# Kernel tuning notes

Measured on AMD Instinct MI355X. Metric: run time of the kernel, lower is better.

The kernel has to match this reference:

```python
import jax, jax.numpy as jnp
import numpy as np

DET = 512       # detector bins
N_THETA = 180   # projection angles, theta = 0..179 degrees (1 deg spacing)


def _ramp_filter(size):
    """skimage _get_fourier_filter(size, 'ramp'): spatial ramp -> FFT."""
    n = np.concatenate((np.arange(1, size // 2 + 1, 2),
                        np.arange(size // 2 - 1, 0, -2)))
    f = np.zeros(size)
    f[0] = 0.25
    f[1::2] = -1.0 / (np.pi * n) ** 2
    return jnp.asarray(2.0 * np.real(np.fft.fft(f)), dtype=jnp.float32)


def _iradon(x):
    B, C, det, A = x.shape
    theta = jnp.deg2rad(jnp.arange(A, dtype=jnp.float32))  # 0..179 deg

    # --- ramp filtering along the detector axis ---
    size = max(64, int(2 ** np.ceil(np.log2(2 * det))))  # 1024 for det=512
    filt = _ramp_filter(size)                            # (size,)
    xp = jnp.pad(x, ((0, 0), (0, 0), (0, size - det), (0, 0)))
    proj_f = jnp.fft.fft(xp, axis=2) * filt[None, None, :, None]
    filtered = jnp.real(jnp.fft.ifft(proj_f, axis=2))[:, :, :det, :]  # (B,C,det,A)

    # --- backprojection (circle=False) ---
    out_size = int(np.floor(np.sqrt(det ** 2 / 2.0)))  # 362
    radius = out_size // 2
    xpr = jnp.arange(out_size, dtype=jnp.float32)[:, None] - radius  # rows
    ypr = jnp.arange(out_size, dtype=jnp.float32)[None, :] - radius  # cols
    cos_t = jnp.cos(theta)
    sin_t = jnp.sin(theta)
    # detector coordinate for every (angle, pixel): t = y*cos - x*sin
    t = ypr[None] * cos_t[:, None, None] - xpr[None] * sin_t[:, None, None]  # (A,out,out)
    pos = t + det // 2          # index into detector axis (x = arange(det)-det//2)
    i0 = jnp.floor(pos).astype(jnp.int32)
    frac = pos - i0.astype(jnp.float32)
    in_range = ((pos >= 0) & (pos <= det - 1)).astype(jnp.float32)  # fill_value=0 outside
    i0c = jnp.clip(i0, 0, det - 1)
    i1c = jnp.clip(i0 + 1, 0, det - 1)

    P = out_size * out_size
    ft = jnp.moveaxis(filtered, 3, 2)                     # (B,C,A,det)
    idx0 = jnp.broadcast_to(i0c.reshape(A, P)[None, None], (B, C, A, P))
    idx1 = jnp.broadcast_to(i1c.reshape(A, P)[None, None], (B, C, A, P))
    g0 = jnp.take_along_axis(ft, idx0, axis=3)            # (B,C,A,P)
    g1 = jnp.take_along_axis(ft, idx1, axis=3)
    w = frac.reshape(A, P)[None, None]
    m = in_range.reshape(A, P)[None, None]
    val = ((1.0 - w) * g0 + w * g1) * m                   # bilinear-in-1D interp, 0 outside
    recon = val.sum(axis=2).reshape(B, C, out_size, out_size)
    return recon * (jnp.pi / (2.0 * A))


def setup_inputs() -> dict:
    key = jax.random.key(0)
    x = jax.random.normal(key, (4, 1, DET, N_THETA), dtype=jnp.float32)
    return {"x": x}


def reference(x):
    return _iradon(x)
```

## Files before the change

### kernel.cpp

```cpp
#include <hip/hip_runtime.h>
#include <math.h>

#define DET 512
#define NA  180
#define OUT 362
#define RAD 181

#define NSPLIT 6
#define APB    30
#define CHUNK  6
#define LSTRIDE 516

constexpr double PI_D = 3.14159265358979323846;

constexpr double tsin(double x) {
    double x2 = x * x;
    return x * (1.0 + x2 * (-1.0/6 + x2 * (1.0/120 + x2 * (-1.0/5040 +
               x2 * (1.0/362880 + x2 * (-1.0/39916800))))));
}
constexpr double tcos(double x) {
    double x2 = x * x;
    return 1.0 + x2 * (-0.5 + x2 * (1.0/24 + x2 * (-1.0/720 +
               x2 * (1.0/40320 + x2 * (-1.0/3628800)))));
}

struct Trig { float c[NA]; float s[NA]; };
constexpr Trig make_trig() {
    Trig t{};
    constexpr double r = PI_D / 180.0;
    for (int k = 0; k < NA; ++k) {
        double c, s;
        if (k <= 45)       { c =  tcos(k * r);          s =  tsin(k * r); }
        else if (k <= 90)  { c =  tsin((90 - k) * r);   s =  tcos((90 - k) * r); }
        else if (k <= 135) { c = -tsin((k - 90) * r);   s =  tcos((k - 90) * r); }
        else               { c = -tcos((180 - k) * r);  s =  tsin((180 - k) * r); }
        t.c[k] = (float)c; t.s[k] = (float)s;
    }
    return t;
}
__device__ constexpr Trig TRIG = make_trig();

__host__ __device__ constexpr float rampw0(int m) {
    int a = m < 0 ? -m : m;
    if (a > 511 || (a & 1) == 0) return 0.0f;
    double md = (double)a;
    return (float)(-2.0 / (PI_D * PI_D * md * md));
}

template<int R>
__device__ __forceinline__ void tap(const float* __restrict__ p,
        float& a0, float& a1, float& a2, float& a3) {
    const float v = p[R];
    if constexpr (rampw0(R)      != 0.0f) a0 = fmaf(rampw0(R),      v, a0);
    if constexpr (rampw0(R - 32) != 0.0f) a1 = fmaf(rampw0(R - 32), v, a1);
    if constexpr (rampw0(R - 64) != 0.0f) a2 = fmaf(rampw0(R - 64), v, a2);
    if constexpr (rampw0(R - 96) != 0.0f) a3 = fmaf(rampw0(R - 96), v, a3);
}

template<int R, int REND>
__device__ __forceinline__ void sweep(const float* __restrict__ p,
        float& a0, float& a1, float& a2, float& a3) {
    if constexpr (R <= REND) {
        tap<R>(p, a0, a1, a2, a3);
        sweep<R + 2, REND>(p, a0, a1, a2, a3);
    }
}

__global__ __launch_bounds__(256) void ramp_filter_kernel(
        const float* __restrict__ x, float* __restrict__ ft) {
    const int a   = blockIdx.x;
    const int b   = blockIdx.y;
    const int tid = threadIdx.x;
    const int t    = tid & 127;
    const int half = tid >> 7;
    const int q = (t & 31) + 128 * (t >> 5);

    __shared__ float xs[3 * DET];
    __shared__ float red[4 * 128];

    xs[tid]        = 0.0f;
    xs[256 + tid]  = 0.0f;
    xs[1024 + tid] = 0.0f;
    xs[1280 + tid] = 0.0f;
    xs[512 + tid]  = x[(b * DET + tid) * NA + a];
    xs[768 + tid]  = x[(b * DET + 256 + tid) * NA + a];
    __syncthreads();

    const float* p = xs + 512 + q;
    float a0 = 0.0f, a1 = 0.0f, a2 = 0.0f, a3 = 0.0f;

    if (half == 0) {
        a0 = 0.5f * p[0];
        a1 = 0.5f * p[32];
        a2 = 0.5f * p[64];
        a3 = 0.5f * p[96];
        sweep<-511, 47>(p, a0, a1, a2, a3);
    } else {
        sweep<49, 607>(p, a0, a1, a2, a3);
        red[      t] = a0;
        red[128 + t] = a1;
        red[256 + t] = a2;
        red[384 + t] = a3;
    }
    __syncthreads();

    if (half == 0) {
        float* o = ft + (b * NA + a) * DET + q;
        o[0]  = a0 + red[      t];
        o[32] = a1 + red[128 + t];
        o[64] = a2 + red[256 + t];
        o[96] = a3 + red[384 + t];
    }
}

__device__ __forceinline__ float interp1(const float* __restrict__ L, float pos) {
    float pf = floorf(pos);
    int   i0 = (int)pf;
    float fr = pos - pf;
    float g0 = L[i0];
    float g1 = L[i0 + 1];
    float v  = fmaf(fr, g1 - g0, g0);
    return pos <= (float)(DET - 1) ? v : 0.0f;
}

__global__ __launch_bounds__(256, 8) void backproject_kernel(
        const float* __restrict__ ft, float* __restrict__ out) {
    const int bz = blockIdx.z;
    const int b  = bz / NSPLIT;
    const int sp = bz - b * NSPLIT;
    const int r0 = blockIdx.y * 32;
    const int c0 = blockIdx.x * 32;
    const int tid = threadIdx.x;
    const int tx = tid & 15;
    const int ty = tid >> 4;

    __shared__ float line[CHUNK * LSTRIDE];

    if (tid < CHUNK) line[tid * LSTRIDE + 512] = 0.0f;

    const float xpr = (float)(min(r0 + ty, OUT - 1) - RAD);
    const float ypr = (float)(min(c0 + tx, OUT - 1) - RAD);

    float a00 = 0.0f, a01 = 0.0f, a10 = 0.0f, a11 = 0.0f;

    const float* base = ft + (b * NA + sp * APB) * DET;

    for (int rd = 0; rd < APB / CHUNK; ++rd) {
        __syncthreads();
        const float4* g = (const float4*)(base + rd * CHUNK * DET);
        #pragma unroll
        for (int k = 0; k < (CHUNK * DET / 4) / 256; ++k) {
            int j4 = tid + k * 256;
            float4 v = g[j4];
            int c = j4 >> 7;
            int d = (j4 & 127) << 2;
            *(float4*)&line[c * LSTRIDE + d] = v;
        }
        __syncthreads();

        const int abase = sp * APB + rd * CHUNK;
        #pragma unroll
        for (int i = 0; i < CHUNK; ++i) {
            const float cv = TRIG.c[abase + i];
            const float sv = TRIG.s[abase + i];
            float p00 = fmaf(ypr, cv, fmaf(xpr, -sv, 256.0f));
            float p01 = fmaf(16.0f, cv, p00);
            float p10 = fmaf(-16.0f, sv, p00);
            float p11 = fmaf(-16.0f, sv, p01);
            const float* L = line + i * LSTRIDE;
            a00 += interp1(L, p00);
            a01 += interp1(L, p01);
            a10 += interp1(L, p10);
            a11 += interp1(L, p11);
        }
    }

    const float scale = (float)(PI_D / (2.0 * NA));
    const int r = r0 + ty;
    const int c = c0 + tx;
    float* ob = out + b * OUT * OUT;
    if (r < OUT) {
        if (c < OUT)      atomicAdd(&ob[r * OUT + c],      a00 * scale);
        if (c + 16 < OUT) atomicAdd(&ob[r * OUT + c + 16], a01 * scale);
    }
    if (r + 16 < OUT) {
        if (c < OUT)      atomicAdd(&ob[(r + 16) * OUT + c],      a10 * scale);
        if (c + 16 < OUT) atomicAdd(&ob[(r + 16) * OUT + c + 16], a11 * scale);
    }
}

extern "C" void kernel_launch(void* const* d_in, const int* in_sizes, int n_in,
                              void* d_out, int out_size, void* d_ws, size_t ws_size,
                              hipStream_t stream) {
    const float* x = (const float*)d_in[0];
    float* ft  = (float*)d_ws;
    float* out = (float*)d_out;

    const int B = in_sizes[0] / (DET * NA);

    hipMemsetAsync(out, 0, (size_t)out_size * sizeof(float), stream);
    ramp_filter_kernel<<<dim3(NA, B), 256, 0, stream>>>(x, ft);
    backproject_kernel<<<dim3((OUT + 31) / 32, (OUT + 31) / 32, B * NSPLIT),
                         256, 0, stream>>>(ft, out);
}
```

Baseline: 98.49 us.

## Interleave batch into float4 detector lines and split ramp filter four ways

The filtered sinogram is now stored batch-interleaved as float4 (angle, detector, batch), so each backprojection thread computes its interpolation position and index once and serves all four batch images with one 16-byte LDS load per tap. The angle split grows to 12 blocks per tile (each with 15 angles in chunks of 5), and the batch dimension leaves the grid. The ramp filter moves to 512 threads, splitting the tap sweep into four quarters with a three-way shared reduction. In exchange the batch size is hardcoded to 4, accumulator and LDS pressure rise, and the out-of-range check now redirects loads to a zero-padded slot.

```diff
diff --git a/kernel.cpp b/kernel.cpp
--- a/kernel.cpp
+++ b/kernel.cpp
@@ -5,11 +5,13 @@
 #define NA  180
 #define OUT 362
 #define RAD 181
-
-#define NSPLIT 6
-#define APB    30
-#define CHUNK  6
-#define LSTRIDE 516
+#define OUTSQ (OUT * OUT)
+#define NB  4
+
+#define NSPLIT 12
+#define APB    15
+#define CHUNK  5
+#define LQ     514
 
 constexpr double PI_D = 3.14159265358979323846;
 
@@ -66,95 +68,97 @@
     }
 }
 
-__global__ __launch_bounds__(256) void ramp_filter_kernel(
+__global__ __launch_bounds__(512) void ramp_filter_kernel(
         const float* __restrict__ x, float* __restrict__ ft) {
     const int a   = blockIdx.x;
     const int b   = blockIdx.y;
     const int tid = threadIdx.x;
-    const int t    = tid & 127;
-    const int half = tid >> 7;
+    const int t   = tid & 127;
+    const int qtr = tid >> 7;
     const int q = (t & 31) + 128 * (t >> 5);
 
     __shared__ float xs[3 * DET];
-    __shared__ float red[4 * 128];
+    __shared__ float red[3][4][128];
 
     xs[tid]        = 0.0f;
-    xs[256 + tid]  = 0.0f;
     xs[1024 + tid] = 0.0f;
-    xs[1280 + tid] = 0.0f;
     xs[512 + tid]  = x[(b * DET + tid) * NA + a];
-    xs[768 + tid]  = x[(b * DET + 256 + tid) * NA + a];
     __syncthreads();
 
     const float* p = xs + 512 + q;
     float a0 = 0.0f, a1 = 0.0f, a2 = 0.0f, a3 = 0.0f;
 
-    if (half == 0) {
+    if (qtr == 0) {
         a0 = 0.5f * p[0];
         a1 = 0.5f * p[32];
         a2 = 0.5f * p[64];
         a3 = 0.5f * p[96];
-        sweep<-511, 47>(p, a0, a1, a2, a3);
+        sweep<-511, -233>(p, a0, a1, a2, a3);
+    } else if (qtr == 1) {
+        sweep<-231, 47>(p, a0, a1, a2, a3);
+    } else if (qtr == 2) {
+        sweep<49, 327>(p, a0, a1, a2, a3);
     } else {
-        sweep<49, 607>(p, a0, a1, a2, a3);
-        red[      t] = a0;
-        red[128 + t] = a1;
-        red[256 + t] = a2;
-        red[384 + t] = a3;
+        sweep<329, 607>(p, a0, a1, a2, a3);
+    }
+    if (qtr != 0) {
+        red[qtr - 1][0][t] = a0;
+        red[qtr - 1][1][t] = a1;
+        red[qtr - 1][2][t] = a2;
+        red[qtr - 1][3][t] = a3;
     }
     __syncthreads();
 
-    if (half == 0) {
-        float* o = ft + (b * NA + a) * DET + q;
-        o[0]  = a0 + red[      t];
-        o[32] = a1 + red[128 + t];
-        o[64] = a2 + red[256 + t];
-        o[96] = a3 + red[384 + t];
-    }
-}
-
-__device__ __forceinline__ float interp1(const float* __restrict__ L, float pos) {
+    if (qtr == 0) {
+        float* ob = ft + ((size_t)a * DET + q) * NB + b;
+        ob[0 * 4 * NB / 4 * 0] = 0.0f;
+        ob[0]        = a0 + red[0][0][t] + red[1][0][t] + red[2][0][t];
+        ob[32 * NB]  = a1 + red[0][1][t] + red[1][1][t] + red[2][1][t];
+        ob[64 * NB]  = a2 + red[0][2][t] + red[1][2][t] + red[2][2][t];
+        ob[96 * NB]  = a3 + red[0][3][t] + red[1][3][t] + red[2][3][t];
+    }
+}
+
+__device__ __forceinline__ void acc4(float4& acc,
+        const float4* __restrict__ L, float pos) {
     float pf = floorf(pos);
+    float fr = pos - pf;
     int   i0 = (int)pf;
-    float fr = pos - pf;
-    float g0 = L[i0];
-    float g1 = L[i0 + 1];
-    float v  = fmaf(fr, g1 - g0, g0);
-    return pos <= (float)(DET - 1) ? v : 0.0f;
-}
-
-__global__ __launch_bounds__(256, 8) void backproject_kernel(
-        const float* __restrict__ ft, float* __restrict__ out) {
-    const int bz = blockIdx.z;
-    const int b  = bz / NSPLIT;
-    const int sp = bz - b * NSPLIT;
+    const float4* q = (pos > (float)(DET - 1)) ? (L + DET) : (L + i0);
+    float4 g0 = q[0];
+    float4 g1 = q[1];
+    acc.x += fmaf(fr, g1.x - g0.x, g0.x);
+    acc.y += fmaf(fr, g1.y - g0.y, g0.y);
+    acc.z += fmaf(fr, g1.z - g0.z, g0.z);
+    acc.w += fmaf(fr, g1.w - g0.w, g0.w);
+}
+
+__global__ __launch_bounds__(256) void backproject_kernel(
+        const float4* __restrict__ ftq, float* __restrict__ out) {
+    const int sp = blockIdx.z;
     const int r0 = blockIdx.y * 32;
     const int c0 = blockIdx.x * 32;
     const int tid = threadIdx.x;
     const int tx = tid & 15;
     const int ty = tid >> 4;
 
-    __shared__ float line[CHUNK * LSTRIDE];
-
-    if (tid < CHUNK) line[tid * LSTRIDE + 512] = 0.0f;
+    __shared__ float4 lines[CHUNK][LQ];
+
+    if (tid < 2 * CHUNK)
+        lines[tid >> 1][DET + (tid & 1)] = float4{0.0f, 0.0f, 0.0f, 0.0f};
 
     const float xpr = (float)(min(r0 + ty, OUT - 1) - RAD);
     const float ypr = (float)(min(c0 + tx, OUT - 1) - RAD);
 
-    float a00 = 0.0f, a01 = 0.0f, a10 = 0.0f, a11 = 0.0f;
-
-    const float* base = ft + (b * NA + sp * APB) * DET;
+    float4 a00 = {0,0,0,0}, a01 = {0,0,0,0}, a10 = {0,0,0,0}, a11 = {0,0,0,0};
 
     for (int rd = 0; rd < APB / CHUNK; ++rd) {
         __syncthreads();
-        const float4* g = (const float4*)(base + rd * CHUNK * DET);
+        const float4* g = ftq + (size_t)(sp * APB + rd * CHUNK) * DET;
         #pragma unroll
-        for (int k = 0; k < (CHUNK * DET / 4) / 256; ++k) {
-            int j4 = tid + k * 256;
-            float4 v = g[j4];
-            int c = j4 >> 7;
-            int d = (j4 & 127) << 2;
-            *(float4*)&line[c * LSTRIDE + d] = v;
+        for (int k = 0; k < CHUNK * DET / 256; ++k) {
+            int j = tid + k * 256;
+            lines[j >> 9][j & 511] = g[j];
         }
         __syncthreads();
 
@@ -167,26 +171,31 @@
             float p01 = fmaf(16.0f, cv, p00);
             float p10 = fmaf(-16.0f, sv, p00);
             float p11 = fmaf(-16.0f, sv, p01);
-            const float* L = line + i * LSTRIDE;
-            a00 += interp1(L, p00);
-            a01 += interp1(L, p01);
-            a10 += interp1(L, p10);
-            a11 += interp1(L, p11);
+            const float4* L = &lines[i][0];
+            acc4(a00, L, p00);
+            acc4(a01, L, p01);
+            acc4(a10, L, p10);
+            acc4(a11, L, p11);
         }
     }
 
     const float scale = (float)(PI_D / (2.0 * NA));
     const int r = r0 + ty;
     const int c = c0 + tx;
-    float* ob = out + b * OUT * OUT;
-    if (r < OUT) {
-        if (c < OUT)      atomicAdd(&ob[r * OUT + c],      a00 * scale);
-        if (c + 16 < OUT) atomicAdd(&ob[r * OUT + c + 16], a01 * scale);
-    }
-    if (r + 16 < OUT) {
-        if (c < OUT)      atomicAdd(&ob[(r + 16) * OUT + c],      a10 * scale);
-        if (c + 16 < OUT) atomicAdd(&ob[(r + 16) * OUT + c + 16], a11 * scale);
-    }
+
+#define EMIT(ACC, RR, CC)                                          \
+    if ((RR) < OUT && (CC) < OUT) {                                \
+        const int off = (RR) * OUT + (CC);                         \
+        atomicAdd(out + off,             (ACC).x * scale);         \
+        atomicAdd(out + OUTSQ + off,     (ACC).y * scale);         \
+        atomicAdd(out + 2 * OUTSQ + off, (ACC).z * scale);         \
+        atomicAdd(out + 3 * OUTSQ + off, (ACC).w * scale);         \
+    }
+    EMIT(a00, r, c);
+    EMIT(a01, r, c + 16);
+    EMIT(a10, r + 16, c);
+    EMIT(a11, r + 16, c + 16);
+#undef EMIT
 }
 
 extern "C" void kernel_launch(void* const* d_in, const int* in_sizes, int n_in,
@@ -199,7 +208,7 @@
     const int B = in_sizes[0] / (DET * NA);
 
     hipMemsetAsync(out, 0, (size_t)out_size * sizeof(float), stream);
-    ramp_filter_kernel<<<dim3(NA, B), 256, 0, stream>>>(x, ft);
-    backproject_kernel<<<dim3((OUT + 31) / 32, (OUT + 31) / 32, B * NSPLIT),
-                         256, 0, stream>>>(ft, out);
-}
+    ramp_filter_kernel<<<dim3(NA, B), 512, 0, stream>>>(x, ft);
+    backproject_kernel<<<dim3((OUT + 31) / 32, (OUT + 31) / 32, NSPLIT),
+                         256, 0, stream>>>((const float4*)ft, out);
+}
```

Result: slower. 107.6 us (+9.3%).

## Enlarge backprojection tile to 4x4 pixels per thread and split angles finer

Applied to the files above, without the earlier changes.

Each thread now accumulates a 4x4 pixel micro-tile (a 64x64 block tile) instead of 2x2. The angle range is split 18 ways instead of 6, with 10 angles per block loaded 5 per chunk. The larger tile amortizes the shared-memory line loads and trig setup over more pixels per block, and the finer split keeps the grid large enough to fill the GPU. In exchange it uses more registers, has more partially idle edge tiles, and triples the atomicAdd traffic to the output.

```diff
diff --git a/kernel.cpp b/kernel.cpp
--- a/kernel.cpp
+++ b/kernel.cpp
@@ -5,10 +5,11 @@
 #define NA  180
 #define OUT 362
 #define RAD 181
-
-#define NSPLIT 6
-#define APB    30
-#define CHUNK  6
+#define OUTSQ (OUT * OUT)
+
+#define NSPLIT 18
+#define APB    10
+#define CHUNK  5
 #define LSTRIDE 516
 
 constexpr double PI_D = 3.14159265358979323846;
@@ -105,7 +106,7 @@
     __syncthreads();
 
     if (half == 0) {
-        float* o = ft + (b * NA + a) * DET + q;
+        float* o = ft + ((size_t)b * NA + a) * DET + q;
         o[0]  = a0 + red[      t];
         o[32] = a1 + red[128 + t];
         o[64] = a2 + red[256 + t];
@@ -123,13 +124,13 @@
     return pos <= (float)(DET - 1) ? v : 0.0f;
 }
 
-__global__ __launch_bounds__(256, 8) void backproject_kernel(
+__global__ __launch_bounds__(256) void backproject_kernel(
         const float* __restrict__ ft, float* __restrict__ out) {
     const int bz = blockIdx.z;
     const int b  = bz / NSPLIT;
     const int sp = bz - b * NSPLIT;
-    const int r0 = blockIdx.y * 32;
-    const int c0 = blockIdx.x * 32;
+    const int r0 = blockIdx.y * 64;
+    const int c0 = blockIdx.x * 64;
     const int tid = threadIdx.x;
     const int tx = tid & 15;
     const int ty = tid >> 4;
@@ -138,23 +139,33 @@
 
     if (tid < CHUNK) line[tid * LSTRIDE + 512] = 0.0f;
 
-    const float xpr = (float)(min(r0 + ty, OUT - 1) - RAD);
-    const float ypr = (float)(min(c0 + tx, OUT - 1) - RAD);
-
-    float a00 = 0.0f, a01 = 0.0f, a10 = 0.0f, a11 = 0.0f;
-
-    const float* base = ft + (b * NA + sp * APB) * DET;
+    float xr[4], yc[4];
+    #pragma unroll
+    for (int k = 0; k < 4; ++k) {
+        xr[k] = (float)(min(r0 + ty + 16 * k, OUT - 1) - RAD);
+        yc[k] = (float)(min(c0 + tx + 16 * k, OUT - 1) - RAD);
+    }
+
+    float acc[4][4];
+    #pragma unroll
+    for (int r = 0; r < 4; ++r)
+        #pragma unroll
+        for (int c = 0; c < 4; ++c) acc[r][c] = 0.0f;
+
+    const float* base = ft + ((size_t)b * NA + sp * APB) * DET;
 
     for (int rd = 0; rd < APB / CHUNK; ++rd) {
         __syncthreads();
         const float4* g = (const float4*)(base + rd * CHUNK * DET);
         #pragma unroll
-        for (int k = 0; k < (CHUNK * DET / 4) / 256; ++k) {
+        for (int k = 0; k < (CHUNK * DET / 4 + 255) / 256; ++k) {
             int j4 = tid + k * 256;
-            float4 v = g[j4];
-            int c = j4 >> 7;
-            int d = (j4 & 127) << 2;
-            *(float4*)&line[c * LSTRIDE + d] = v;
+            if (j4 < CHUNK * DET / 4) {
+                float4 v = g[j4];
+                int cl = j4 >> 7;
+                int d  = (j4 & 127) << 2;
+                *(float4*)&line[cl * LSTRIDE + d] = v;
+            }
         }
         __syncthreads();
 
@@ -163,29 +174,34 @@
         for (int i = 0; i < CHUNK; ++i) {
             const float cv = TRIG.c[abase + i];
             const float sv = TRIG.s[abase + i];
-            float p00 = fmaf(ypr, cv, fmaf(xpr, -sv, 256.0f));
-            float p01 = fmaf(16.0f, cv, p00);
-            float p10 = fmaf(-16.0f, sv, p00);
-            float p11 = fmaf(-16.0f, sv, p01);
             const float* L = line + i * LSTRIDE;
-            a00 += interp1(L, p00);
-            a01 += interp1(L, p01);
-            a10 += interp1(L, p10);
-            a11 += interp1(L, p11);
+            float pr[4];
+            #pragma unroll
+            for (int r = 0; r < 4; ++r) pr[r] = fmaf(xr[r], -sv, 256.0f);
+            #pragma unroll
+            for (int r = 0; r < 4; ++r) {
+                #pragma unroll
+                for (int c = 0; c < 4; ++c) {
+                    float p = fmaf(yc[c], cv, pr[r]);
+                    acc[r][c] += interp1(L, p);
+                }
+            }
         }
     }
 
     const float scale = (float)(PI_D / (2.0 * NA));
-    const int r = r0 + ty;
-    const int c = c0 + tx;
-    float* ob = out + b * OUT * OUT;
-    if (r < OUT) {
-        if (c < OUT)      atomicAdd(&ob[r * OUT + c],      a00 * scale);
-        if (c + 16 < OUT) atomicAdd(&ob[r * OUT + c + 16], a01 * scale);
-    }
-    if (r + 16 < OUT) {
-        if (c < OUT)      atomicAdd(&ob[(r + 16) * OUT + c],      a10 * scale);
-        if (c + 16 < OUT) atomicAdd(&ob[(r + 16) * OUT + c + 16], a11 * scale);
+    float* ob = out + (size_t)b * OUTSQ;
+    #pragma unroll
+    for (int r = 0; r < 4; ++r) {
+        const int rr = r0 + ty + 16 * r;
+        if (rr < OUT) {
+            #pragma unroll
+            for (int c = 0; c < 4; ++c) {
+                const int cc = c0 + tx + 16 * c;
+                if (cc < OUT)
+                    atomicAdd(&ob[rr * OUT + cc], acc[r][c] * scale);
+            }
+        }
     }
 }
 
@@ -200,6 +216,6 @@
 
     hipMemsetAsync(out, 0, (size_t)out_size * sizeof(float), stream);
     ramp_filter_kernel<<<dim3(NA, B), 256, 0, stream>>>(x, ft);
-    backproject_kernel<<<dim3((OUT + 31) / 32, (OUT + 31) / 32, B * NSPLIT),
+    backproject_kernel<<<dim3((OUT + 63) / 64, (OUT + 63) / 64, B * NSPLIT),
                          256, 0, stream>>>(ft, out);
 }
```

Measured after the change: 259.2 us. 163% more time.

## Interleave batch pairs in filtered sinogram so backprojection shares coordinate math

Applied to the files above, without the earlier changes.

The ramp filter now writes its output with two batch images interleaved per detector bin. Each backprojection block then handles two images at once, so the position, floor and fraction work is computed once and used for two interpolations. The LDS chunk is halved to keep the shared memory footprint the same, and the grid is halved in z. The launch-bounds occupancy hint is dropped. This assumes B is even and roughly doubles accumulator registers.

```diff
diff --git a/kernel.cpp b/kernel.cpp
--- a/kernel.cpp
+++ b/kernel.cpp
@@ -5,11 +5,12 @@
 #define NA  180
 #define OUT 362
 #define RAD 181
+#define OUTSQ (OUT * OUT)
 
 #define NSPLIT 6
 #define APB    30
-#define CHUNK  6
-#define LSTRIDE 516
+#define CHUNK  3
+#define LSTR2  1028
 
 constexpr double PI_D = 3.14159265358979323846;
 
@@ -105,56 +106,63 @@
     __syncthreads();
 
     if (half == 0) {
-        float* o = ft + (b * NA + a) * DET + q;
-        o[0]  = a0 + red[      t];
-        o[32] = a1 + red[128 + t];
-        o[64] = a2 + red[256 + t];
-        o[96] = a3 + red[384 + t];
-    }
-}
-
-__device__ __forceinline__ float interp1(const float* __restrict__ L, float pos) {
+        const int g = b >> 1, j = b & 1;
+        float* o = ft + (((size_t)g * NA + a) * DET + q) * 2 + j;
+        o[0]       = a0 + red[      t];
+        o[32 * 2]  = a1 + red[128 + t];
+        o[64 * 2]  = a2 + red[256 + t];
+        o[96 * 2]  = a3 + red[384 + t];
+    }
+}
+
+__device__ __forceinline__ void interp2(float2& acc,
+        const float* __restrict__ L, float pos) {
     float pf = floorf(pos);
     int   i0 = (int)pf;
     float fr = pos - pf;
-    float g0 = L[i0];
-    float g1 = L[i0 + 1];
-    float v  = fmaf(fr, g1 - g0, g0);
-    return pos <= (float)(DET - 1) ? v : 0.0f;
-}
-
-__global__ __launch_bounds__(256, 8) void backproject_kernel(
-        const float* __restrict__ ft, float* __restrict__ out) {
+    const float* qp = L + 2 * i0;
+    float g00 = qp[0], g01 = qp[1];
+    float g10 = qp[2], g11 = qp[3];
+    float v0 = fmaf(fr, g10 - g00, g00);
+    float v1 = fmaf(fr, g11 - g01, g01);
+    bool in = pos <= (float)(DET - 1);
+    acc.x += in ? v0 : 0.0f;
+    acc.y += in ? v1 : 0.0f;
+}
+
+__global__ __launch_bounds__(256) void backproject_kernel(
+        const float* __restrict__ ftp, float* __restrict__ out) {
     const int bz = blockIdx.z;
-    const int b  = bz / NSPLIT;
-    const int sp = bz - b * NSPLIT;
+    const int g  = bz / NSPLIT;
+    const int sp = bz - g * NSPLIT;
     const int r0 = blockIdx.y * 32;
     const int c0 = blockIdx.x * 32;
     const int tid = threadIdx.x;
     const int tx = tid & 15;
     const int ty = tid >> 4;
 
-    __shared__ float line[CHUNK * LSTRIDE];
-
-    if (tid < CHUNK) line[tid * LSTRIDE + 512] = 0.0f;
+    __shared__ float line[CHUNK * LSTR2];
+
+    if (tid < 2 * CHUNK)
+        line[(tid >> 1) * LSTR2 + 1024 + (tid & 1)] = 0.0f;
 
     const float xpr = (float)(min(r0 + ty, OUT - 1) - RAD);
     const float ypr = (float)(min(c0 + tx, OUT - 1) - RAD);
 
-    float a00 = 0.0f, a01 = 0.0f, a10 = 0.0f, a11 = 0.0f;
-
-    const float* base = ft + (b * NA + sp * APB) * DET;
+    float2 a00 = {0,0}, a01 = {0,0}, a10 = {0,0}, a11 = {0,0};
+
+    const float* base = ftp + ((size_t)g * NA + sp * APB) * DET * 2;
 
     for (int rd = 0; rd < APB / CHUNK; ++rd) {
         __syncthreads();
-        const float4* g = (const float4*)(base + rd * CHUNK * DET);
+        const float4* gq = (const float4*)(base + rd * CHUNK * DET * 2);
         #pragma unroll
-        for (int k = 0; k < (CHUNK * DET / 4) / 256; ++k) {
+        for (int k = 0; k < CHUNK * DET * 2 / 4 / 256; ++k) {
             int j4 = tid + k * 256;
-            float4 v = g[j4];
-            int c = j4 >> 7;
-            int d = (j4 & 127) << 2;
-            *(float4*)&line[c * LSTRIDE + d] = v;
+            float4 v = gq[j4];
+            int cl = j4 >> 8;
+            int d  = (j4 & 255) << 2;
+            *(float4*)&line[cl * LSTR2 + d] = v;
         }
         __syncthreads();
 
@@ -167,26 +175,31 @@
             float p01 = fmaf(16.0f, cv, p00);
             float p10 = fmaf(-16.0f, sv, p00);
             float p11 = fmaf(-16.0f, sv, p01);
-            const float* L = line + i * LSTRIDE;
-            a00 += interp1(L, p00);
-            a01 += interp1(L, p01);
-            a10 += interp1(L, p10);
-            a11 += interp1(L, p11);
+            const float* L = line + i * LSTR2;
+            interp2(a00, L, p00);
+            interp2(a01, L, p01);
+            interp2(a10, L, p10);
+            interp2(a11, L, p11);
         }
     }
 
     const float scale = (float)(PI_D / (2.0 * NA));
     const int r = r0 + ty;
     const int c = c0 + tx;
-    float* ob = out + b * OUT * OUT;
-    if (r < OUT) {
-        if (c < OUT)      atomicAdd(&ob[r * OUT + c],      a00 * scale);
-        if (c + 16 < OUT) atomicAdd(&ob[r * OUT + c + 16], a01 * scale);
-    }
-    if (r + 16 < OUT) {
-        if (c < OUT)      atomicAdd(&ob[(r + 16) * OUT + c],      a10 * scale);
-        if (c + 16 < OUT) atomicAdd(&ob[(r + 16) * OUT + c + 16], a11 * scale);
-    }
+    float* ob0 = out + (size_t)(2 * g)     * OUTSQ;
+    float* ob1 = out + (size_t)(2 * g + 1) * OUTSQ;
+
+#define EMIT(ACC, RR, CC)                                          \
+    if ((RR) < OUT && (CC) < OUT) {                                \
+        const int off = (RR) * OUT + (CC);                         \
+        atomicAdd(ob0 + off, (ACC).x * scale);                     \
+        atomicAdd(ob1 + off, (ACC).y * scale);                     \
+    }
+    EMIT(a00, r, c);
+    EMIT(a01, r, c + 16);
+    EMIT(a10, r + 16, c);
+    EMIT(a11, r + 16, c + 16);
+#undef EMIT
 }
 
 extern "C" void kernel_launch(void* const* d_in, const int* in_sizes, int n_in,
@@ -200,6 +213,6 @@
 
     hipMemsetAsync(out, 0, (size_t)out_size * sizeof(float), stream);
     ramp_filter_kernel<<<dim3(NA, B), 256, 0, stream>>>(x, ft);
-    backproject_kernel<<<dim3((OUT + 31) / 32, (OUT + 31) / 32, B * NSPLIT),
+    backproject_kernel<<<dim3((OUT + 31) / 32, (OUT + 31) / 32, (B / 2) * NSPLIT),
                          256, 0, stream>>>(ft, out);
 }
```

Result: no change. 97.85 us (-0.6%).
